# Kernel optimization log

Hardware: AMD Instinct MI355X
Metric: run time of the kernel (lower is better)

Reference implementation:

```python
import jax, jax.numpy as jnp
import numpy as np

H = 768            # hidden_size
I = 384            # moe_intermediate_size
E = 16             # n_routed_experts
G = 4              # n_group
TOPK_GROUP = 2
TOP_K = 4
SCALE = 2.5        # routed_scaling_factor
N_SHARED = 2
IS = I * N_SHARED  # shared expert intermediate
B, S = 1, 2048


def setup_inputs() -> dict:
    key = jax.random.key(0)
    ks = jax.random.split(key, 16)
    s = lambda k, shape, fan: jax.random.normal(k, shape, jnp.float32) * (fan ** -0.5)
    return {
        'hidden_states': jax.random.normal(ks[0], (B, S, H), jnp.float32),
        # router
        'router_w': s(ks[1], (E, H), H),
        'router_b': jnp.zeros((E,), jnp.float32),
        'corr_bias': jnp.zeros((E,), jnp.float32),
        # routed experts, stacked [E, ...]
        'gWg': s(ks[2], (E, H, I), H),
        'gbg': jnp.zeros((E, I), jnp.float32),
        'gWu': s(ks[3], (E, H, I), H),
        'gbu': jnp.zeros((E, I), jnp.float32),
        'gWd': s(ks[4], (E, I, H), I),
        'gbd': jnp.zeros((E, H), jnp.float32),
        # shared expert
        'sWg': s(ks[5], (H, IS), H),
        'sbg': jnp.zeros((IS,), jnp.float32),
        'sWu': s(ks[6], (H, IS), H),
        'sbu': jnp.zeros((IS,), jnp.float32),
        'sWd': s(ks[7], (IS, H), IS),
        'sbd': jnp.zeros((H,), jnp.float32),
    }


def _route(x, router_w, router_b, corr_bias):
    # x: [T, H] -> topk_indices [T, K], topk_weights [T, K]
    logits = x.astype(jnp.float32) @ router_w.T + router_b          # [T, E]
    scores = jax.nn.sigmoid(logits)
    sfc = scores + corr_bias[None, :]                                # [T, E]
    # group scores: sum of top-2 per group
    grp = sfc.reshape(-1, G, E // G)
    group_scores = jax.lax.top_k(grp, 2)[0].sum(-1)                  # [T, G]
    _, gidx = jax.lax.top_k(group_scores, TOPK_GROUP)                # [T, topk_group]
    gmask = jax.nn.one_hot(gidx, G, dtype=sfc.dtype).sum(axis=1)     # [T, G]
    score_mask = jnp.repeat(gmask, E // G, axis=-1)                  # [T, E]
    sfc = jnp.where(score_mask > 0, sfc, 0.0)
    _, idx = jax.lax.top_k(sfc, TOP_K)                               # [T, K]
    w = jnp.take_along_axis(scores, idx, axis=1)                     # [T, K]
    w = w / (w.sum(-1, keepdims=True) + 1e-20)                       # norm_topk_prob
    return idx, w * SCALE


def reference(hidden_states, router_w, router_b, corr_bias,
              gWg, ggbg, gWu, gbu, gWd, gbd,
              sWg, sbg, sWu, sbu, sWd, sbd):
    # note: arg name gbg kept consistent below
    return _forward(hidden_states, router_w, router_b, corr_bias,
                    gWg, gbg_fix(gWg, gbg := gbg_dummy()), gWu, gbu, gWd, gbd,
                    sWg, sbg, sWu, sbu, sWd, sbd)


# --- real implementation (the above placeholder is replaced here) ---

def _forward(x3, router_w, router_b, corr_bias, gWg, gbg, gWu, gbu, gWd, gbd,
             sWg, sbg, sWu, sbu, sWd, sbd):
    orig_shape = x3.shape
    x = x3.reshape(-1, H)                                            # [T, H]
    idx, w = _route(x, router_w, router_b, corr_bias)
    # combine weights per (token, expert): zero for non-selected experts
    c = (jax.nn.one_hot(idx, E, dtype=w.dtype) * w[..., None]).sum(1)  # [T, E]
    # all-expert gated MLP (zero combine weight => zero contribution)
    h = jax.nn.silu(jnp.einsum('th,ehi->tei', x, gWg) + gbg) * \
        (jnp.einsum('th,ehi->tei', x, gWu) + gbu)                    # [T, E, I]
    out_e = jnp.einsum('tei,eih->teh', h, gWd) + gbd                 # [T, E, H]
    moe_out = jnp.einsum('te,teh->th', c, out_e)                     # [T, H]
    # shared experts on the residual input
    hs = jax.nn.silu(x @ sWg + sbg) * (x @ sWu + sbu)
    shared = hs @ sWd + sbd
    return (moe_out + shared).reshape(orig_shape)


def reference(hidden_states, router_w, router_b, corr_bias,
              gWg, gbg, gWu, gbu, gWd, gbd,
              sWg, sbg, sWu, sbu, sWd, sbd):
    return _forward(hidden_states, router_w, router_b, corr_bias,
                    gWg, gbg, gWu, gbu, gWd, gbd,
                    sWg, sbg, sWu, sbu, sWd, sbd)
```

## Files before the change

### kernel.cpp

```cpp
#include <hip/hip_runtime.h>
#include <hip/hip_bf16.h>
#include <math.h>

#define H 768
#define I_DIM 384
#define E_NUM 16
#define G_NUM 4
#define TOPK 4
#define IS_DIM 768
#define SCALE_F 2.5f

#define BM 128
#define BK 32
#define LDA 40

typedef __attribute__((ext_vector_type(8))) __bf16 bf16x8;
typedef __attribute__((ext_vector_type(4))) float f32x4;

static __device__ __forceinline__ unsigned short f2bf(float f) {
    __bf16 h = (__bf16)f;
    return __builtin_bit_cast(unsigned short, h);
}

static __device__ __forceinline__ int swz8(int row, int c) {
    return row * LDA + (((c ^ (row >> 3)) & 3) << 3);
}

__global__ __launch_bounds__(256) void router_score_k(
    const float* __restrict__ X, const float* __restrict__ RW,
    const float* __restrict__ RB, const float* __restrict__ CB,
    int* __restrict__ sel_out, float* __restrict__ w_out, int T)
{
    const int wid = threadIdx.x >> 6;
    const int lane = threadIdx.x & 63;
    const int t = blockIdx.x * 4 + wid;
    const int e = lane & 15;
    const int chunk = lane >> 4;
    const float* xr = X + (size_t)t * H + chunk * (H / 4);
    const float* wr = RW + (size_t)e * H + chunk * (H / 4);
    float s = 0.f;
#pragma unroll 4
    for (int j = 0; j < H / 4; j += 4) {
        float4 a = *(const float4*)(xr + j);
        float4 b = *(const float4*)(wr + j);
        s += a.x * b.x + a.y * b.y + a.z * b.z + a.w * b.w;
    }
    s += __shfl_xor(s, 16);
    s += __shfl_xor(s, 32);

    __shared__ float sc_s[4][E_NUM];
    __shared__ float sf_s[4][E_NUM];
    if (lane < E_NUM) {
        float logit = s + RB[e];
        float score = 1.f / (1.f + expf(-logit));
        sc_s[wid][e] = score;
        sf_s[wid][e] = score + CB[e];
    }
    __syncthreads();

    if (lane == 0) {
        float gs[G_NUM];
        for (int g = 0; g < G_NUM; ++g) {
            float m1 = -1e30f, m2 = -1e30f;
            for (int j = 0; j < E_NUM / G_NUM; ++j) {
                float v = sf_s[wid][g * (E_NUM / G_NUM) + j];
                if (v > m1) { m2 = m1; m1 = v; }
                else if (v > m2) { m2 = v; }
            }
            gs[g] = m1 + m2;
        }
        int g1 = 0;
        for (int g = 1; g < G_NUM; ++g) if (gs[g] > gs[g1]) g1 = g;
        int g2 = -1;
        for (int g = 0; g < G_NUM; ++g) {
            if (g == g1) continue;
            if (g2 < 0 || gs[g] > gs[g2]) g2 = g;
        }
        float m[E_NUM];
        for (int i = 0; i < E_NUM; ++i) {
            int g = i >> 2;
            m[i] = (g == g1 || g == g2) ? sf_s[wid][i] : 0.f;
        }
        float wsum = 0.f;
        int sel[TOPK]; float wv[TOPK];
        for (int k = 0; k < TOPK; ++k) {
            int best = 0; float bv = -1e30f;
            for (int i = 0; i < E_NUM; ++i)
                if (m[i] > bv) { bv = m[i]; best = i; }
            m[best] = -2e30f;
            sel[k] = best;
            wv[k] = sc_s[wid][best];
            wsum += wv[k];
        }
        float inv = SCALE_F / (wsum + 1e-20f);
        int4 so = { sel[0], sel[1], sel[2], sel[3] };
        float4 wo = { wv[0] * inv, wv[1] * inv, wv[2] * inv, wv[3] * inv };
        *(int4*)&sel_out[(size_t)t * 4] = so;
        *(float4*)&w_out[(size_t)t * 4] = wo;
    }
}

__global__ __launch_bounds__(256) void build_lists_k(
    const int* __restrict__ sel, const float* __restrict__ wv,
    int* __restrict__ cnt, int* __restrict__ tok_id, float* __restrict__ tok_w,
    int T)
{
    const int e = blockIdx.x;
    const int tid = threadIdx.x;
    const int wid = tid >> 6, lane = tid & 63;
    __shared__ int wtot[4];
    __shared__ int base_s;
    if (tid == 0) base_s = 0;
    __syncthreads();

    for (int t0 = 0; t0 < T; t0 += 256) {
        const int t = t0 + tid;
        int flag = 0; float myw = 0.f;
        int4 sv = *(const int4*)&sel[(size_t)t * 4];
        float4 wq = *(const float4*)&wv[(size_t)t * 4];
        if (sv.x == e) { flag = 1; myw = wq.x; }
        if (sv.y == e) { flag = 1; myw = wq.y; }
        if (sv.z == e) { flag = 1; myw = wq.z; }
        if (sv.w == e) { flag = 1; myw = wq.w; }
        unsigned long long mb = __ballot(flag);
        if (lane == 0) wtot[wid] = __popcll(mb);
        __syncthreads();
        int wo = 0;
#pragma unroll
        for (int q = 0; q < 4; ++q) if (q < wid) wo += wtot[q];
        const int stot = wtot[0] + wtot[1] + wtot[2] + wtot[3];
        const int mypos = base_s + wo + __popcll(mb & ((1ull << lane) - 1ull));
        if (flag) {
            tok_id[(size_t)e * T + mypos] = t;
            tok_w[(size_t)e * T + mypos] = myw;
        }
        __syncthreads();
        if (tid == 0) base_s += stot;
    }
    __syncthreads();
    if (tid == 0) cnt[e] = base_s;
}

__global__ void scan_k(const int* __restrict__ cnt, int* __restrict__ offs)
{
    if (threadIdx.x == 0) {
        int a = 0;
        for (int e2 = 0; e2 < E_NUM; ++e2) { offs[e2] = a; a += cnt[e2]; }
        offs[E_NUM] = a;
    }
}

__global__ __launch_bounds__(256) void cvtx_k(
    const float* __restrict__ src, unsigned short* __restrict__ dst, int n8)
{
    int i = blockIdx.x * 256 + threadIdx.x;
    if (i >= n8) return;
    const float4* s = (const float4*)(src + (size_t)i * 8);
    float4 a = s[0], b = s[1];
    unsigned short u[8] = { f2bf(a.x), f2bf(a.y), f2bf(a.z), f2bf(a.w),
                            f2bf(b.x), f2bf(b.y), f2bf(b.z), f2bf(b.w) };
    *(uint4*)(dst + (size_t)i * 8) = *(uint4*)u;
}

static __device__ __forceinline__ void wr4(
    unsigned short* Bt, int n, int kr, float4 v)
{
    const int cg = kr >> 3, kl = kr & 7;
    Bt[(n + 0) * LDA + (((cg ^ ((n + 0) >> 3)) & 3) << 3) + kl] = f2bf(v.x);
    Bt[(n + 1) * LDA + (((cg ^ ((n + 1) >> 3)) & 3) << 3) + kl] = f2bf(v.y);
    Bt[(n + 2) * LDA + (((cg ^ ((n + 2) >> 3)) & 3) << 3) + kl] = f2bf(v.z);
    Bt[(n + 3) * LDA + (((cg ^ ((n + 3) >> 3)) & 3) << 3) + kl] = f2bf(v.w);
}

template<bool GATHER>
__global__ __launch_bounds__(256) void gateup_mfma_k(
    const unsigned short* __restrict__ Xb,
    const float* __restrict__ WgP,
    const float* __restrict__ WuP,
    const float* __restrict__ bgp, const float* __restrict__ bup,
    const int* __restrict__ cnt, const int* __restrict__ offs,
    const int* __restrict__ tok_id,
    unsigned short* __restrict__ HO,
    int T, int NI)
{
    const int e = GATHER ? blockIdx.z : 0;
    const int ne = GATHER ? cnt[e] : T;
    const int m0 = blockIdx.x * BM;
    if (m0 >= ne) return;
    const int n0 = blockIdx.y * 64;

    const float* Wg = WgP + (GATHER ? (size_t)e * H * NI : 0);
    const float* Wu = WuP + (GATHER ? (size_t)e * H * NI : 0);
    const float* bg = bgp + (GATHER ? e * NI : 0);
    const float* bu = bup + (GATHER ? e * NI : 0);
    const int obase = GATHER ? offs[e] : 0;
    const int* tl = tok_id + (GATHER ? (size_t)e * T : 0);

    __shared__ unsigned short Al[BM * LDA];
    __shared__ unsigned short Bgl[64 * LDA];
    __shared__ unsigned short Bul[64 * LDA];

    const int tid = threadIdx.x;
    const int srow = tid >> 2;
    const int sseg = (tid & 3) * 8;
    const int kr0 = tid >> 4;
    const int c4 = (tid & 15) * 4;

    int r0i = m0 + srow, r1i = m0 + srow + 64;
    if (GATHER) { r0i = min(r0i, ne - 1); r1i = min(r1i, ne - 1); }
    const int tok0 = GATHER ? tl[r0i] : r0i;
    const int tok1 = GATHER ? tl[r1i] : r1i;
    const unsigned short* a0p = Xb + (size_t)tok0 * H + sseg;
    const unsigned short* a1p = Xb + (size_t)tok1 * H + sseg;

    const int lane = tid & 63;
    const int wid = tid >> 6;
    const int wr = wid >> 1, wc = wid & 1;
    const int lrow = lane & 15;
    const int lkc = lane >> 4;

    f32x4 accg[4][2] = {};
    f32x4 accu[4][2] = {};

    for (int k0 = 0; k0 < H; k0 += BK) {
        uint4 av0 = *(const uint4*)(a0p + k0);
        uint4 av1 = *(const uint4*)(a1p + k0);
        float4 gv0 = *(const float4*)(Wg + (size_t)(k0 + kr0) * NI + n0 + c4);
        float4 gv1 = *(const float4*)(Wg + (size_t)(k0 + kr0 + 16) * NI + n0 + c4);
        float4 uv0 = *(const float4*)(Wu + (size_t)(k0 + kr0) * NI + n0 + c4);
        float4 uv1 = *(const float4*)(Wu + (size_t)(k0 + kr0 + 16) * NI + n0 + c4);
        __syncthreads();
        *(uint4*)&Al[swz8(srow, tid & 3)] = av0;
        *(uint4*)&Al[swz8(srow + 64, tid & 3)] = av1;
        wr4(Bgl, c4, kr0, gv0);
        wr4(Bgl, c4, kr0 + 16, gv1);
        wr4(Bul, c4, kr0, uv0);
        wr4(Bul, c4, kr0 + 16, uv1);
        __syncthreads();
        bf16x8 af[4], gf[2], uf[2];
#pragma unroll
        for (int i = 0; i < 4; ++i)
            af[i] = *(const bf16x8*)&Al[swz8(wr * 64 + i * 16 + lrow, lkc)];
#pragma unroll
        for (int j = 0; j < 2; ++j) {
            gf[j] = *(const bf16x8*)&Bgl[swz8(wc * 32 + j * 16 + lrow, lkc)];
            uf[j] = *(const bf16x8*)&Bul[swz8(wc * 32 + j * 16 + lrow, lkc)];
        }
#pragma unroll
        for (int i = 0; i < 4; ++i)
#pragma unroll
            for (int j = 0; j < 2; ++j) {
                accg[i][j] = __builtin_amdgcn_mfma_f32_16x16x32_bf16(af[i], gf[j], accg[i][j], 0, 0, 0);
                accu[i][j] = __builtin_amdgcn_mfma_f32_16x16x32_bf16(af[i], uf[j], accu[i][j], 0, 0, 0);
            }
    }

    const int q4 = (lane >> 4) * 4;
    const int cc = lane & 15;
#pragma unroll
    for (int i = 0; i < 4; ++i)
#pragma unroll
        for (int j = 0; j < 2; ++j)
#pragma unroll
            for (int r = 0; r < 4; ++r) {
                const int row = m0 + wr * 64 + i * 16 + q4 + r;
                if (!GATHER || row < ne) {
                    const int col = n0 + wc * 32 + j * 16 + cc;
                    float g = accg[i][j][r] + bg[col];
                    float u = accu[i][j][r] + bu[col];
                    float s = g / (1.f + expf(-g)) * u;
                    HO[(size_t)(obase + row) * NI + col] = f2bf(s);
                }
            }
}

template<bool SCATTER>
__global__ __launch_bounds__(256) void down_mfma_k(
    const unsigned short* __restrict__ Hb,
    const float* __restrict__ WdP,
    const float* __restrict__ bdp,
    const int* __restrict__ cnt, const int* __restrict__ offs,
    const int* __restrict__ tok_id, const float* __restrict__ tok_w,
    float* __restrict__ OUT, int T, int K)
{
    const int e = SCATTER ? blockIdx.z : 0;
    const int ne = SCATTER ? cnt[e] : T;
    const int m0 = blockIdx.x * BM;
    if (m0 >= ne) return;
    const int n0 = blockIdx.y * 128;

    const float* Wd = WdP + (SCATTER ? (size_t)e * K * H : 0);
    const float* bd = bdp + (SCATTER ? e * H : 0);
    const int abase = SCATTER ? offs[e] : 0;

    __shared__ unsigned short Al[BM * LDA];
    __shared__ unsigned short Bl[128 * LDA];

    const int tid = threadIdx.x;
    const int srow = tid >> 2;
    const int sseg = (tid & 3) * 8;
    const int kr0 = tid >> 5;
    const int c4 = (tid & 31) * 4;

    const int r0i = min(m0 + srow, ne - 1);
    const int r1i = min(m0 + srow + 64, ne - 1);
    const unsigned short* a0p = Hb + (size_t)(abase + r0i) * K + sseg;
    const unsigned short* a1p = Hb + (size_t)(abase + r1i) * K + sseg;

    const int lane = tid & 63;
    const int wid = tid >> 6;
    const int wr = wid >> 1, wc = wid & 1;
    const int lrow = lane & 15;
    const int lkc = lane >> 4;

    f32x4 acc[4][4] = {};

    for (int k0 = 0; k0 < K; k0 += BK) {
        uint4 av0 = *(const uint4*)(a0p + k0);
        uint4 av1 = *(const uint4*)(a1p + k0);
        float4 bv0 = *(const float4*)(Wd + (size_t)(k0 + kr0) * H + n0 + c4);
        float4 bv1 = *(const float4*)(Wd + (size_t)(k0 + kr0 + 8) * H + n0 + c4);
        float4 bv2 = *(const float4*)(Wd + (size_t)(k0 + kr0 + 16) * H + n0 + c4);
        float4 bv3 = *(const float4*)(Wd + (size_t)(k0 + kr0 + 24) * H + n0 + c4);
        __syncthreads();
        *(uint4*)&Al[swz8(srow, tid & 3)] = av0;
        *(uint4*)&Al[swz8(srow + 64, tid & 3)] = av1;
        wr4(Bl, c4, kr0, bv0);
        wr4(Bl, c4, kr0 + 8, bv1);
        wr4(Bl, c4, kr0 + 16, bv2);
        wr4(Bl, c4, kr0 + 24, bv3);
        __syncthreads();
        bf16x8 af[4], bfr[4];
#pragma unroll
        for (int i = 0; i < 4; ++i) {
            af[i]  = *(const bf16x8*)&Al[swz8(wr * 64 + i * 16 + lrow, lkc)];
            bfr[i] = *(const bf16x8*)&Bl[swz8(wc * 64 + i * 16 + lrow, lkc)];
        }
#pragma unroll
        for (int i = 0; i < 4; ++i)
#pragma unroll
            for (int j = 0; j < 4; ++j)
                acc[i][j] = __builtin_amdgcn_mfma_f32_16x16x32_bf16(af[i], bfr[j], acc[i][j], 0, 0, 0);
    }

    const int q4 = (lane >> 4) * 4;
    const int cc = lane & 15;
#pragma unroll
    for (int i = 0; i < 4; ++i) {
        const int rbase = m0 + wr * 64 + i * 16 + q4;
        if (SCATTER) {
#pragma unroll
            for (int r = 0; r < 4; ++r) {
                const int row = rbase + r;
                if (row < ne) {
                    const int tok = tok_id[(size_t)e * T + row];
                    const float w = tok_w[(size_t)e * T + row];
#pragma unroll
                    for (int j = 0; j < 4; ++j) {
                        const int col = n0 + wc * 64 + j * 16 + cc;
                        atomicAdd(&OUT[(size_t)tok * H + col], w * (acc[i][j][r] + bd[col]));
                    }
                }
            }
        } else {
#pragma unroll
            for (int r = 0; r < 4; ++r) {
                const int row = rbase + r;
#pragma unroll
                for (int j = 0; j < 4; ++j) {
                    const int col = n0 + wc * 64 + j * 16 + cc;
                    OUT[(size_t)row * H + col] = acc[i][j][r] + bd[col];
                }
            }
        }
    }
}

extern "C" void kernel_launch(void* const* d_in, const int* in_sizes, int n_in,
                              void* d_out, int out_size, void* d_ws, size_t ws_size,
                              hipStream_t stream)
{
    const float* X   = (const float*)d_in[0];
    const float* RW  = (const float*)d_in[1];
    const float* RB  = (const float*)d_in[2];
    const float* CB  = (const float*)d_in[3];
    const float* GWg = (const float*)d_in[4];
    const float* Gbg = (const float*)d_in[5];
    const float* GWu = (const float*)d_in[6];
    const float* Gbu = (const float*)d_in[7];
    const float* GWd = (const float*)d_in[8];
    const float* Gbd = (const float*)d_in[9];
    const float* SWg = (const float*)d_in[10];
    const float* Sbg = (const float*)d_in[11];
    const float* SWu = (const float*)d_in[12];
    const float* Sbu = (const float*)d_in[13];
    const float* SWd = (const float*)d_in[14];
    const float* Sbd = (const float*)d_in[15];
    float* OUT = (float*)d_out;
    const int T = in_sizes[0] / H;

    char* w = (char*)d_ws;
    int* cnt     = (int*)w;            w += 256;
    int* offs    = (int*)w;            w += 256;
    int* sel     = (int*)w;            w += (size_t)T * TOPK * sizeof(int);
    float* selw  = (float*)w;          w += (size_t)T * TOPK * sizeof(float);
    int* tok_id  = (int*)w;            w += (size_t)E_NUM * T * sizeof(int);
    float* tok_w = (float*)w;          w += (size_t)E_NUM * T * sizeof(float);
    unsigned short* Xb = (unsigned short*)w; w += (size_t)T * H * 2;
    unsigned short* HSs = (unsigned short*)w;
    unsigned short* HBr = (unsigned short*)w; w += (size_t)T * TOPK * I_DIM * 2;

    router_score_k<<<T / 4, 256, 0, stream>>>(X, RW, RB, CB, sel, selw, T);
    build_lists_k<<<E_NUM, 256, 0, stream>>>(sel, selw, cnt, tok_id, tok_w, T);
    scan_k<<<1, 64, 0, stream>>>(cnt, offs);
    cvtx_k<<<(T * H / 8 + 255) / 256, 256, 0, stream>>>(X, Xb, T * H / 8);

    gateup_mfma_k<false><<<dim3(T / BM, IS_DIM / 64, 1), 256, 0, stream>>>(
        Xb, SWg, SWu, Sbg, Sbu, nullptr, nullptr, nullptr, HSs, T, IS_DIM);
    down_mfma_k<false><<<dim3(T / BM, H / 128, 1), 256, 0, stream>>>(
        HSs, SWd, Sbd, nullptr, nullptr, nullptr, nullptr, OUT, T, IS_DIM);

    gateup_mfma_k<true><<<dim3(T / BM, I_DIM / 64, E_NUM), 256, 0, stream>>>(
        Xb, GWg, GWu, Gbg, Gbu, cnt, offs, tok_id, HBr, T, I_DIM);
    down_mfma_k<true><<<dim3(T / BM, H / 128, E_NUM), 256, 0, stream>>>(
        HBr, GWd, Gbd, cnt, offs, tok_id, tok_w, OUT, T, I_DIM);
}
```

Before: 362.5 us.

## Fuse bf16 conversion into router, merge gate-up launches, prefetch next K tile

The fp32-to-bf16 conversion of X moves into the router kernel, which already reads each token row, so the separate conversion launch goes away. The shared and routed gate-up GEMMs become a single launch with an extra z slice for the shared expert, so one launch fills the GPU instead of two. Both GEMM kernels now issue the global loads for the next K tile right after the LDS barrier, overlapping them with the MFMAs. In exchange, the shared and routed hidden buffers get separate workspace regions, register pressure rises from the prefetch, and the merged grid launches many blocks that exit early.

Measured after the change: 347.4 us. 4.2% less time.

```diff
diff --git a/kernel.cpp b/kernel.cpp
--- a/kernel.cpp
+++ b/kernel.cpp
@@ -29,7 +29,8 @@
 __global__ __launch_bounds__(256) void router_score_k(
     const float* __restrict__ X, const float* __restrict__ RW,
     const float* __restrict__ RB, const float* __restrict__ CB,
-    int* __restrict__ sel_out, float* __restrict__ w_out, int T)
+    int* __restrict__ sel_out, float* __restrict__ w_out,
+    unsigned short* __restrict__ Xb, int T)
 {
     const int wid = threadIdx.x >> 6;
     const int lane = threadIdx.x & 63;
@@ -48,6 +49,17 @@
     s += __shfl_xor(s, 16);
     s += __shfl_xor(s, 32);
 
+    {
+        const float* xrow = X + (size_t)t * H;
+        unsigned short* brow = Xb + (size_t)t * H;
+#pragma unroll
+        for (int p = 0; p < 3; ++p) {
+            float4 v = *(const float4*)(xrow + p * 256 + lane * 4);
+            ushort4 o = { f2bf(v.x), f2bf(v.y), f2bf(v.z), f2bf(v.w) };
+            *(ushort4*)(brow + p * 256 + lane * 4) = o;
+        }
+    }
+
     __shared__ float sc_s[4][E_NUM];
     __shared__ float sf_s[4][E_NUM];
     if (lane < E_NUM) {
@@ -150,18 +162,6 @@
     }
 }
 
-__global__ __launch_bounds__(256) void cvtx_k(
-    const float* __restrict__ src, unsigned short* __restrict__ dst, int n8)
-{
-    int i = blockIdx.x * 256 + threadIdx.x;
-    if (i >= n8) return;
-    const float4* s = (const float4*)(src + (size_t)i * 8);
-    float4 a = s[0], b = s[1];
-    unsigned short u[8] = { f2bf(a.x), f2bf(a.y), f2bf(a.z), f2bf(a.w),
-                            f2bf(b.x), f2bf(b.y), f2bf(b.z), f2bf(b.w) };
-    *(uint4*)(dst + (size_t)i * 8) = *(uint4*)u;
-}
-
 static __device__ __forceinline__ void wr4(
     unsigned short* Bt, int n, int kr, float4 v)
 {
@@ -172,29 +172,34 @@
     Bt[(n + 3) * LDA + (((cg ^ ((n + 3) >> 3)) & 3) << 3) + kl] = f2bf(v.w);
 }
 
-template<bool GATHER>
-__global__ __launch_bounds__(256) void gateup_mfma_k(
+__global__ __launch_bounds__(256) void gateup_all_k(
     const unsigned short* __restrict__ Xb,
-    const float* __restrict__ WgP,
-    const float* __restrict__ WuP,
-    const float* __restrict__ bgp, const float* __restrict__ bup,
+    const float* __restrict__ GWg, const float* __restrict__ GWu,
+    const float* __restrict__ Gbg, const float* __restrict__ Gbu,
+    const float* __restrict__ SWg, const float* __restrict__ SWu,
+    const float* __restrict__ Sbg, const float* __restrict__ Sbu,
     const int* __restrict__ cnt, const int* __restrict__ offs,
     const int* __restrict__ tok_id,
-    unsigned short* __restrict__ HO,
-    int T, int NI)
-{
-    const int e = GATHER ? blockIdx.z : 0;
-    const int ne = GATHER ? cnt[e] : T;
+    unsigned short* __restrict__ HBr,
+    unsigned short* __restrict__ HSs,
+    int T)
+{
+    const int z = blockIdx.z;
+    const bool SH = (z == E_NUM);
+    const int NI = SH ? IS_DIM : I_DIM;
+    const int n0 = blockIdx.y * 64;
+    if (n0 >= NI) return;
+    const int ne = SH ? T : cnt[z];
     const int m0 = blockIdx.x * BM;
     if (m0 >= ne) return;
-    const int n0 = blockIdx.y * 64;
-
-    const float* Wg = WgP + (GATHER ? (size_t)e * H * NI : 0);
-    const float* Wu = WuP + (GATHER ? (size_t)e * H * NI : 0);
-    const float* bg = bgp + (GATHER ? e * NI : 0);
-    const float* bu = bup + (GATHER ? e * NI : 0);
-    const int obase = GATHER ? offs[e] : 0;
-    const int* tl = tok_id + (GATHER ? (size_t)e * T : 0);
+
+    const float* Wg = SH ? SWg : GWg + (size_t)z * H * I_DIM;
+    const float* Wu = SH ? SWu : GWu + (size_t)z * H * I_DIM;
+    const float* bg = SH ? Sbg : Gbg + z * I_DIM;
+    const float* bu = SH ? Sbu : Gbu + z * I_DIM;
+    unsigned short* HO = SH ? HSs : HBr;
+    const int obase = SH ? 0 : offs[z];
+    const int* tl = tok_id + (size_t)z * T;
 
     __shared__ unsigned short Al[BM * LDA];
     __shared__ unsigned short Bgl[64 * LDA];
@@ -207,28 +212,32 @@
     const int c4 = (tid & 15) * 4;
 
     int r0i = m0 + srow, r1i = m0 + srow + 64;
-    if (GATHER) { r0i = min(r0i, ne - 1); r1i = min(r1i, ne - 1); }
-    const int tok0 = GATHER ? tl[r0i] : r0i;
-    const int tok1 = GATHER ? tl[r1i] : r1i;
+    if (!SH) { r0i = min(r0i, ne - 1); r1i = min(r1i, ne - 1); }
+    const int tok0 = SH ? r0i : tl[r0i];
+    const int tok1 = SH ? r1i : tl[r1i];
     const unsigned short* a0p = Xb + (size_t)tok0 * H + sseg;
     const unsigned short* a1p = Xb + (size_t)tok1 * H + sseg;
 
     const int lane = tid & 63;
-    const int wid = tid >> 6;
-    const int wr = wid >> 1, wc = wid & 1;
+    const int wvid = tid >> 6;
+    const int wr = wvid >> 1, wc = wvid & 1;
     const int lrow = lane & 15;
     const int lkc = lane >> 4;
 
     f32x4 accg[4][2] = {};
     f32x4 accu[4][2] = {};
 
+    uint4 av0, av1; float4 gv0, gv1, uv0, uv1;
+#define GU_LOADS(K)                                                        \
+    av0 = *(const uint4*)(a0p + (K));                                      \
+    av1 = *(const uint4*)(a1p + (K));                                      \
+    gv0 = *(const float4*)(Wg + (size_t)((K) + kr0) * NI + n0 + c4);       \
+    gv1 = *(const float4*)(Wg + (size_t)((K) + kr0 + 16) * NI + n0 + c4);  \
+    uv0 = *(const float4*)(Wu + (size_t)((K) + kr0) * NI + n0 + c4);       \
+    uv1 = *(const float4*)(Wu + (size_t)((K) + kr0 + 16) * NI + n0 + c4);
+
+    GU_LOADS(0);
     for (int k0 = 0; k0 < H; k0 += BK) {
-        uint4 av0 = *(const uint4*)(a0p + k0);
-        uint4 av1 = *(const uint4*)(a1p + k0);
-        float4 gv0 = *(const float4*)(Wg + (size_t)(k0 + kr0) * NI + n0 + c4);
-        float4 gv1 = *(const float4*)(Wg + (size_t)(k0 + kr0 + 16) * NI + n0 + c4);
-        float4 uv0 = *(const float4*)(Wu + (size_t)(k0 + kr0) * NI + n0 + c4);
-        float4 uv1 = *(const float4*)(Wu + (size_t)(k0 + kr0 + 16) * NI + n0 + c4);
         __syncthreads();
         *(uint4*)&Al[swz8(srow, tid & 3)] = av0;
         *(uint4*)&Al[swz8(srow + 64, tid & 3)] = av1;
@@ -237,6 +246,7 @@
         wr4(Bul, c4, kr0, uv0);
         wr4(Bul, c4, kr0 + 16, uv1);
         __syncthreads();
+        if (k0 + BK < H) { GU_LOADS(k0 + BK); }
         bf16x8 af[4], gf[2], uf[2];
 #pragma unroll
         for (int i = 0; i < 4; ++i)
@@ -254,6 +264,7 @@
                 accu[i][j] = __builtin_amdgcn_mfma_f32_16x16x32_bf16(af[i], uf[j], accu[i][j], 0, 0, 0);
             }
     }
+#undef GU_LOADS
 
     const int q4 = (lane >> 4) * 4;
     const int cc = lane & 15;
@@ -264,7 +275,7 @@
 #pragma unroll
             for (int r = 0; r < 4; ++r) {
                 const int row = m0 + wr * 64 + i * 16 + q4 + r;
-                if (!GATHER || row < ne) {
+                if (SH || row < ne) {
                     const int col = n0 + wc * 32 + j * 16 + cc;
                     float g = accg[i][j][r] + bg[col];
                     float u = accu[i][j][r] + bu[col];
@@ -308,20 +319,24 @@
     const unsigned short* a1p = Hb + (size_t)(abase + r1i) * K + sseg;
 
     const int lane = tid & 63;
-    const int wid = tid >> 6;
-    const int wr = wid >> 1, wc = wid & 1;
+    const int wvid = tid >> 6;
+    const int wr = wvid >> 1, wc = wvid & 1;
     const int lrow = lane & 15;
     const int lkc = lane >> 4;
 
     f32x4 acc[4][4] = {};
 
+    uint4 av0, av1; float4 bv0, bv1, bv2, bv3;
+#define DN_LOADS(K0)                                                        \
+    av0 = *(const uint4*)(a0p + (K0));                                      \
+    av1 = *(const uint4*)(a1p + (K0));                                      \
+    bv0 = *(const float4*)(Wd + (size_t)((K0) + kr0) * H + n0 + c4);        \
+    bv1 = *(const float4*)(Wd + (size_t)((K0) + kr0 + 8) * H + n0 + c4);    \
+    bv2 = *(const float4*)(Wd + (size_t)((K0) + kr0 + 16) * H + n0 + c4);   \
+    bv3 = *(const float4*)(Wd + (size_t)((K0) + kr0 + 24) * H + n0 + c4);
+
+    DN_LOADS(0);
     for (int k0 = 0; k0 < K; k0 += BK) {
-        uint4 av0 = *(const uint4*)(a0p + k0);
-        uint4 av1 = *(const uint4*)(a1p + k0);
-        float4 bv0 = *(const float4*)(Wd + (size_t)(k0 + kr0) * H + n0 + c4);
-        float4 bv1 = *(const float4*)(Wd + (size_t)(k0 + kr0 + 8) * H + n0 + c4);
-        float4 bv2 = *(const float4*)(Wd + (size_t)(k0 + kr0 + 16) * H + n0 + c4);
-        float4 bv3 = *(const float4*)(Wd + (size_t)(k0 + kr0 + 24) * H + n0 + c4);
         __syncthreads();
         *(uint4*)&Al[swz8(srow, tid & 3)] = av0;
         *(uint4*)&Al[swz8(srow + 64, tid & 3)] = av1;
@@ -330,6 +345,7 @@
         wr4(Bl, c4, kr0 + 16, bv2);
         wr4(Bl, c4, kr0 + 24, bv3);
         __syncthreads();
+        if (k0 + BK < K) { DN_LOADS(k0 + BK); }
         bf16x8 af[4], bfr[4];
 #pragma unroll
         for (int i = 0; i < 4; ++i) {
@@ -342,6 +358,7 @@
             for (int j = 0; j < 4; ++j)
                 acc[i][j] = __builtin_amdgcn_mfma_f32_16x16x32_bf16(af[i], bfr[j], acc[i][j], 0, 0, 0);
     }
+#undef DN_LOADS
 
     const int q4 = (lane >> 4) * 4;
     const int cc = lane & 15;
@@ -406,22 +423,21 @@
     float* selw  = (float*)w;          w += (size_t)T * TOPK * sizeof(float);
     int* tok_id  = (int*)w;            w += (size_t)E_NUM * T * sizeof(int);
     float* tok_w = (float*)w;          w += (size_t)E_NUM * T * sizeof(float);
-    unsigned short* Xb = (unsigned short*)w; w += (size_t)T * H * 2;
-    unsigned short* HSs = (unsigned short*)w;
+    unsigned short* Xb  = (unsigned short*)w; w += (size_t)T * H * 2;
+    unsigned short* HSs = (unsigned short*)w; w += (size_t)T * IS_DIM * 2;
     unsigned short* HBr = (unsigned short*)w; w += (size_t)T * TOPK * I_DIM * 2;
 
-    router_score_k<<<T / 4, 256, 0, stream>>>(X, RW, RB, CB, sel, selw, T);
+    router_score_k<<<T / 4, 256, 0, stream>>>(X, RW, RB, CB, sel, selw, Xb, T);
     build_lists_k<<<E_NUM, 256, 0, stream>>>(sel, selw, cnt, tok_id, tok_w, T);
     scan_k<<<1, 64, 0, stream>>>(cnt, offs);
-    cvtx_k<<<(T * H / 8 + 255) / 256, 256, 0, stream>>>(X, Xb, T * H / 8);
-
-    gateup_mfma_k<false><<<dim3(T / BM, IS_DIM / 64, 1), 256, 0, stream>>>(
-        Xb, SWg, SWu, Sbg, Sbu, nullptr, nullptr, nullptr, HSs, T, IS_DIM);
+
+    gateup_all_k<<<dim3(T / BM, IS_DIM / 64, E_NUM + 1), 256, 0, stream>>>(
+        Xb, GWg, GWu, Gbg, Gbu, SWg, SWu, Sbg, Sbu,
+        cnt, offs, tok_id, HBr, HSs, T);
+
     down_mfma_k<false><<<dim3(T / BM, H / 128, 1), 256, 0, stream>>>(
         HSs, SWd, Sbd, nullptr, nullptr, nullptr, nullptr, OUT, T, IS_DIM);
 
-    gateup_mfma_k<true><<<dim3(T / BM, I_DIM / 64, E_NUM), 256, 0, stream>>>(
-        Xb, GWg, GWu, Gbg, Gbu, cnt, offs, tok_id, HBr, T, I_DIM);
     down_mfma_k<true><<<dim3(T / BM, H / 128, E_NUM), 256, 0, stream>>>(
         HBr, GWd, Gbd, cnt, offs, tok_id, tok_w, OUT, T, I_DIM);
 }
```
